# Kernel tuning notes

Measured on AMD Instinct MI355X. Metric: run time of the kernel, lower is better.

Reference implementation:

```python
import jax, jax.numpy as jnp
import numpy as np

B, T, D = 4, 8192, 1024
H = 16
HD = D // H  # 64
TOP_K = 64


def setup_inputs() -> dict:
    key = jax.random.key(0)
    ks = jax.random.split(key, 6)
    x = jax.random.normal(ks[0], (B, T, D), dtype=jnp.float32)
    # torch nn.Linear weights are [out, in]; y = x @ W.T
    Wq = jax.random.normal(ks[1], (D, D), dtype=jnp.float32) * 0.02
    Wk = jax.random.normal(ks[2], (D, D), dtype=jnp.float32) * 0.02
    Wv = jax.random.normal(ks[3], (D, D), dtype=jnp.float32) * 0.02
    Wo = jax.random.normal(ks[4], (D, D), dtype=jnp.float32) * 0.02
    # indexer: nn.Linear(head_dim, 1, bias=False) -> weight [1, HD]; keep as [HD]
    w_score = jax.random.normal(ks[5], (HD,), dtype=jnp.float32) * 0.02
    return {"x": x, "Wq": Wq, "Wk": Wk, "Wv": Wv, "Wo": Wo, "w_score": w_score}


def reference(x, Wq, Wk, Wv, Wo, w_score):
    b, t, d = x.shape
    top_k = min(TOP_K, t)
    # projections: [B,T,D] -> [B,H,T,HD]
    def proj(W):
        return jnp.einsum('btd,ed->bte', x, W).reshape(b, t, H, HD).transpose(0, 2, 1, 3)
    q = proj(Wq)
    k = proj(Wk)
    v = proj(Wv)
    # lightning indexer scores: [B,H,T]
    idx_scores = jnp.einsum('bhtd,d->bht', k, w_score)
    _, top_idx = jax.lax.top_k(idx_scores, top_k)  # [B,H,K]
    idx = top_idx[..., None]  # [B,H,K,1]
    k_sparse = jnp.take_along_axis(k, idx, axis=2)  # [B,H,K,HD]
    v_sparse = jnp.take_along_axis(v, idx, axis=2)
    scale = HD ** -0.5
    scores = jnp.einsum('bhtd,bhkd->bhtk', q, k_sparse) * scale  # [B,H,T,K]
    attn = jax.nn.softmax(scores, axis=-1)
    out = jnp.einsum('bhtk,bhkd->bhtd', attn, v_sparse)  # [B,H,T,HD]
    out = out.transpose(0, 2, 1, 3).reshape(b, t, d)
    return jnp.einsum('btd,ed->bte', out, Wo)
```

## Files before the change

kernel.cpp:

```cpp
#include <hip/hip_runtime.h>
#include <hip/hip_bf16.h>
#include <stdint.h>

#define NB 4
#define NT 8192
#define ND 1024
#define NH 16
#define NHD 64
#define NK 64
#define NM (NB*NT)

typedef __attribute__((ext_vector_type(4))) float f32x4;
typedef __attribute__((ext_vector_type(8))) short s16x8;
typedef const void __attribute__((address_space(1)))* gas1_t;
typedef void __attribute__((address_space(3)))* las3_t;

__device__ __forceinline__ float bf2f(ushort u) {
  union { uint32_t i; float f; } v; v.i = ((uint32_t)u) << 16; return v.f;
}
__device__ __forceinline__ ushort f2bf(float f) {
  union { float f; uint32_t i; } v; v.f = f;
  uint32_t r = v.i + 0x7FFFu + ((v.i >> 16) & 1u);
  return (ushort)(r >> 16);
}
__device__ __forceinline__ uint32_t f2ord(uint32_t u) {
  return (u & 0x80000000u) ? ~u : (u | 0x80000000u);
}

__global__ __launch_bounds__(256) void convert_w_kernel(
    const float* __restrict__ Wq, const float* __restrict__ Wk,
    const float* __restrict__ Wv, const float* __restrict__ Wo,
    const float* __restrict__ wscore,
    ushort* __restrict__ wqb, ushort* __restrict__ wkb,
    ushort* __restrict__ wvb, ushort* __restrict__ wob,
    ushort* __restrict__ uhi, ushort* __restrict__ ulo) {
  int i = blockIdx.x * 256 + threadIdx.x;
  wqb[i] = f2bf(Wq[i]); wkb[i] = f2bf(Wk[i]);
  wvb[i] = f2bf(Wv[i]); wob[i] = f2bf(Wo[i]);
  if (blockIdx.x < 64) {
    int e = (blockIdx.x & 3) * 256 + threadIdx.x;
    int h = blockIdx.x >> 2;
    float acc = 0.f;
    #pragma unroll 8
    for (int d = 0; d < NHD; ++d) acc += wscore[d] * Wk[(size_t)(h*NHD + d)*ND + e];
    ushort hv = f2bf(acc);
    uhi[h*ND + e] = hv;
    ulo[h*ND + e] = f2bf(acc - bf2f(hv));
  }
}

__global__ __launch_bounds__(256) void prep_x_kernel(
    const float* __restrict__ x, const ushort* __restrict__ uhi,
    const ushort* __restrict__ ulo, ushort* __restrict__ xb,
    float* __restrict__ scores) {
  __shared__ __align__(16) ushort Ahi[32 * 128];
  __shared__ __align__(16) ushort Alo[32 * 128];
  __shared__ float red[4][2][16][17];
  int t = threadIdx.x, w = t >> 6, l = t & 63;
  int tok0 = blockIdx.x * 32;
  int srow = t >> 3;
  int sg = (t & 7) * 2;
  int rs = l & 15, ks8 = (l >> 4) * 8;
  f32x4 acc[2];
  acc[0] = (f32x4){0.f,0.f,0.f,0.f};
  acc[1] = (f32x4){0.f,0.f,0.f,0.f};
  for (int kc = 0; kc < 8; ++kc) {
    int kb = kc * 128;
    {
      const float* xr = x + (size_t)(tok0 + srow) * ND + kb + sg * 8;
      f32x4 v0 = *(const f32x4*)xr;
      f32x4 v1 = *(const f32x4*)(xr + 4);
      f32x4 v2 = *(const f32x4*)(xr + 8);
      f32x4 v3 = *(const f32x4*)(xr + 12);
      s16x8 hi0, lo0, hi1, lo1;
      #pragma unroll
      for (int j = 0; j < 4; ++j) {
        ushort h;
        h = f2bf(v0[j]); hi0[j]   = (short)h; lo0[j]   = (short)f2bf(v0[j] - bf2f(h));
        h = f2bf(v1[j]); hi0[4+j] = (short)h; lo0[4+j] = (short)f2bf(v1[j] - bf2f(h));
        h = f2bf(v2[j]); hi1[j]   = (short)h; lo1[j]   = (short)f2bf(v2[j] - bf2f(h));
        h = f2bf(v3[j]); hi1[4+j] = (short)h; lo1[4+j] = (short)f2bf(v3[j] - bf2f(h));
      }
      ushort* xo = xb + (size_t)(tok0 + srow) * ND + kb + sg * 8;
      *(s16x8*)xo = hi0;
      *(s16x8*)(xo + 8) = hi1;
      int p0 = (sg ^ (srow & 7)) * 8, p1 = ((sg + 1) ^ (srow & 7)) * 8;
      *(s16x8*)&Ahi[srow*128 + p0] = hi0;
      *(s16x8*)&Ahi[srow*128 + p1] = hi1;
      *(s16x8*)&Alo[srow*128 + p0] = lo0;
      *(s16x8*)&Alo[srow*128 + p1] = lo1;
    }
    __syncthreads();
    {
      s16x8 bh = *(const s16x8*)(uhi + rs * ND + kb + w * 32 + ks8);
      s16x8 bl = *(const s16x8*)(ulo + rs * ND + kb + w * 32 + ks8);
      int gl = w * 4 + (l >> 4);
      #pragma unroll
      for (int mi = 0; mi < 2; ++mi) {
        int row = mi * 16 + rs;
        int gp = (gl ^ (row & 7)) * 8;
        s16x8 ah = *(const s16x8*)&Ahi[row*128 + gp];
        s16x8 al = *(const s16x8*)&Alo[row*128 + gp];
        acc[mi] = __builtin_amdgcn_mfma_f32_16x16x32_bf16(ah, bh, acc[mi], 0, 0, 0);
        acc[mi] = __builtin_amdgcn_mfma_f32_16x16x32_bf16(al, bh, acc[mi], 0, 0, 0);
        acc[mi] = __builtin_amdgcn_mfma_f32_16x16x32_bf16(ah, bl, acc[mi], 0, 0, 0);
      }
    }
    __syncthreads();
  }
  #pragma unroll
  for (int mi = 0; mi < 2; ++mi)
    #pragma unroll
    for (int r = 0; r < 4; ++r)
      red[w][mi][(l >> 4) * 4 + r][l & 15] = acc[mi][r];
  __syncthreads();
  int boff = ((tok0 >> 13) << 4);
  int tt0 = tok0 & (NT - 1);
  #pragma unroll
  for (int it = 0; it < 2; ++it) {
    int tok = t & 31, h = (t >> 5) + it * 8;
    int mi = tok >> 4, row = tok & 15;
    float s = red[0][mi][row][h] + red[1][mi][row][h]
            + red[2][mi][row][h] + red[3][mi][row][h];
    scores[(size_t)(boff + h) * NT + tt0 + tok] = s;
  }
}

__global__ __launch_bounds__(256) void topsel_kv_kernel(
    const float* __restrict__ scores, const ushort* __restrict__ xb,
    const ushort* __restrict__ wkb, const ushort* __restrict__ wvb,
    ushort* __restrict__ ksp, ushort* __restrict__ vtsp) {
  int bh = blockIdx.x, t = threadIdx.x;
  int b = bh >> 4, h = bh & 15;
  __shared__ uint32_t keys[NT];
  __shared__ int hist[4096];
  __shared__ uint32_t ck[512];
  __shared__ int ci[512];
  __shared__ int chunksum[256];
  __shared__ int s_binB, s_c0;
  __shared__ int cnt_hi, cnt_cand;
  __shared__ int kid[64];
  __shared__ __align__(16) ushort Xs[64 * 128];
  __shared__ __align__(16) ushort Ws[2][64 * 128];

  for (int i = t; i < 4096; i += 256) hist[i] = 0;
  if (t == 0) { cnt_hi = 0; cnt_cand = 0; }
  __syncthreads();
  const uint4* sg = (const uint4*)(scores + (size_t)bh * NT);
  for (int i = t; i < NT/4; i += 256) {
    uint4 v = sg[i];
    uint32_t k0 = f2ord(v.x), k1 = f2ord(v.y), k2 = f2ord(v.z), k3 = f2ord(v.w);
    keys[i*4+0] = k0; keys[i*4+1] = k1; keys[i*4+2] = k2; keys[i*4+3] = k3;
    atomicAdd(&hist[k0 >> 20], 1); atomicAdd(&hist[k1 >> 20], 1);
    atomicAdd(&hist[k2 >> 20], 1); atomicAdd(&hist[k3 >> 20], 1);
  }
  __syncthreads();
  {
    int hi = 4095 - t * 16;
    int s = 0;
    #pragma unroll
    for (int j = 0; j < 16; ++j) s += hist[hi - j];
    chunksum[t] = s;
  }
  __syncthreads();
  if (t == 0) {
    int cum = 0, c = 0;
    while (cum + chunksum[c] < NK) { cum += chunksum[c]; ++c; }
    int bin = 4095 - c * 16;
    while (cum + hist[bin] < NK) { cum += hist[bin]; --bin; }
    s_binB = bin; s_c0 = cum;
  }
  __syncthreads();
  int binB = s_binB, c0 = s_c0;
  for (int i = t; i < NT; i += 256) {
    int bb = keys[i] >> 20;
    if (bb > binB) {
      int p = atomicAdd(&cnt_hi, 1);
      kid[p] = i;
    } else if (bb == binB) {
      int p = atomicAdd(&cnt_cand, 1);
      if (p < 512) { ck[p] = keys[i]; ci[p] = i; }
    }
  }
  __syncthreads();
  int nc = cnt_cand; if (nc > 512) nc = 512;
  int need = NK - c0;
  for (int p = t; p < nc; p += 256) {
    uint32_t myk = ck[p]; int myi = ci[p];
    int rank = 0;
    for (int j = 0; j < nc; ++j) {
      uint32_t kj = ck[j];
      rank += (kj > myk || (kj == myk && ci[j] < myi)) ? 1 : 0;
    }
    if (rank < need) kid[c0 + rank] = myi;
  }

  int w = t >> 6, l = t & 63;
  int sel = w >> 1, nb = (w & 1) * 32;
  f32x4 acc[4][2];
  #pragma unroll
  for (int mi = 0; mi < 4; ++mi)
    #pragma unroll
    for (int ni = 0; ni < 2; ++ni) acc[mi][ni] = (f32x4){0.f,0.f,0.f,0.f};
  int srow = t >> 2;
  int gj = (t & 3) * 4;
  for (int kc = 0; kc < ND; kc += 128) {
    __syncthreads();
    const ushort* xr  = xb  + (size_t)(b*NT + kid[srow]) * ND + kc;
    const ushort* wkr = wkb + (size_t)(h*NHD + srow) * ND + kc;
    const ushort* wvr = wvb + (size_t)(h*NHD + srow) * ND + kc;
    #pragma unroll
    for (int j = 0; j < 4; ++j) {
      int p = ((gj + j) ^ (srow & 7)) * 8;
      *(uint4*)&Xs[srow*128 + p]    = *(const uint4*)(xr  + (gj + j) * 8);
      *(uint4*)&Ws[0][srow*128 + p] = *(const uint4*)(wkr + (gj + j) * 8);
      *(uint4*)&Ws[1][srow*128 + p] = *(const uint4*)(wvr + (gj + j) * 8);
    }
    __syncthreads();
    #pragma unroll
    for (int ks = 0; ks < 4; ++ks) {
      s16x8 bfr[2], afr[4];
      #pragma unroll
      for (int ni = 0; ni < 2; ++ni) {
        int row = nb + ni*16 + (l & 15);
        bfr[ni] = *(const s16x8*)&Ws[sel][row*128 + ((ks*4 + (l >> 4)) ^ (row & 7))*8];
      }
      #pragma unroll
      for (int mi = 0; mi < 4; ++mi) {
        int row = mi*16 + (l & 15);
        afr[mi] = *(const s16x8*)&Xs[row*128 + ((ks*4 + (l >> 4)) ^ (row & 7))*8];
      }
      #pragma unroll
      for (int mi = 0; mi < 4; ++mi)
        #pragma unroll
        for (int ni = 0; ni < 2; ++ni)
          acc[mi][ni] = __builtin_amdgcn_mfma_f32_16x16x32_bf16(
              afr[mi], bfr[ni], acc[mi][ni], 0, 0, 0);
    }
  }
  #pragma unroll
  for (int mi = 0; mi < 4; ++mi)
    #pragma unroll
    for (int ni = 0; ni < 2; ++ni) {
      int d = nb + ni*16 + (l & 15);
      int key0 = mi*16 + (l >> 4)*4;
      if (sel == 0) {
        #pragma unroll
        for (int r = 0; r < 4; ++r)
          ksp[((size_t)bh*NK + key0 + r)*NHD + d] = f2bf(acc[mi][ni][r]);
      } else {
        ushort4 o;
        o.x = f2bf(acc[mi][ni][0]); o.y = f2bf(acc[mi][ni][1]);
        o.z = f2bf(acc[mi][ni][2]); o.w = f2bf(acc[mi][ni][3]);
        *(ushort4*)&vtsp[((size_t)bh*NHD + d)*NK + key0] = o;
      }
    }
}

template<int STORE_BF16>
__global__ __launch_bounds__(512, 2) void gemm8_kernel(
    const ushort* __restrict__ A, const ushort* __restrict__ Bw,
    void* __restrict__ Cout) {
  __shared__ __align__(16) char lds[131072];
  const int t = threadIdx.x, wid = t >> 6, l = t & 63;
  const int wr = wid >> 2, wc = wid & 3;
  int bid = blockIdx.x;
  int wg = (bid & 7) * 64 + (bid >> 3);
  int tm = wg >> 2, tn = wg & 3;
  const int K = 1024, N = 1024;
  const ushort* Ab = A + (size_t)tm * 256 * K;
  const ushort* Bb = Bw + (size_t)tn * 256 * K;
  const int skh  = ((l & 3) * 8) ^ (((l >> 5) & 1) << 4);
  const int srow = l >> 2;
  const int lane_off = (l & 15) * 64 + ((((l >> 4) * 8) ^ (((l >> 3) & 1) << 4)) * 2);
  f32x4 acc[8][4];
  #pragma unroll
  for (int i = 0; i < 8; ++i)
    #pragma unroll
    for (int j = 0; j < 4; ++j) acc[i][j] = (f32x4){0.f, 0.f, 0.f, 0.f};
  s16x8 afr[4][2], bfr[2][2];

#define STG(gbase, matoff, half, ktile, buf) do { \
    const ushort* _s = (gbase) + (size_t)((half)*128 + wid*16 + srow) * K + (ktile)*64 + skh; \
    int _d = (buf)*65536 + (matoff) + ((half)*128 + wid*16)*64; \
    __builtin_amdgcn_global_load_lds((gas1_t)_s, (las3_t)(lds + _d), 16, 0, 0); \
    __builtin_amdgcn_global_load_lds((gas1_t)(_s + 32), (las3_t)(lds + _d + 16384), 16, 0, 0); \
  } while (0)

#define RD_A(mh, kh, buf) do { \
    _Pragma("unroll") \
    for (int mi = 0; mi < 4; ++mi) \
      afr[mi][kh] = *(const s16x8*)(lds + (buf)*65536 + (kh)*16384 + \
                      ((((mh)*2 + wr)*64 + mi*16))*64 + lane_off); \
  } while (0)

#define RD_B(nh, kh, buf) do { \
    _Pragma("unroll") \
    for (int ni = 0; ni < 2; ++ni) \
      bfr[ni][kh] = *(const s16x8*)(lds + (buf)*65536 + 32768 + (kh)*16384 + \
                      (((nh)*128 + wc*32 + ni*16))*64 + lane_off); \
  } while (0)

#define MMAQH(mh, nh, kh) do { \
    __builtin_amdgcn_s_setprio(1); \
    _Pragma("unroll") \
    for (int mi = 0; mi < 4; ++mi) \
      _Pragma("unroll") \
      for (int ni = 0; ni < 2; ++ni) \
        acc[(mh)*4+mi][(nh)*2+ni] = __builtin_amdgcn_mfma_f32_16x16x32_bf16( \
            afr[mi][kh], bfr[ni][kh], acc[(mh)*4+mi][(nh)*2+ni], 0, 0, 0); \
    __builtin_amdgcn_s_setprio(0); \
  } while (0)

#define LG0() do { asm volatile("s_waitcnt lgkmcnt(0)" ::: "memory"); \
                   __builtin_amdgcn_sched_barrier(0); } while (0)
#define ENDPH() do { __builtin_amdgcn_sched_barrier(0); \
                     __builtin_amdgcn_s_barrier(); } while (0)

#define TILE(kt, bc, bn) do { \
  LG0(); MMAQH(0,0,0); RD_A(0,1,bc); RD_B(0,1,bc); ENDPH(); \
  LG0(); MMAQH(0,0,1); RD_B(1,0,bc); \
  if ((kt)+1 < 16) STG(Bb,32768,0,(kt)+1,bn); ENDPH(); \
  LG0(); MMAQH(0,1,0); RD_B(1,1,bc); ENDPH(); \
  LG0(); MMAQH(0,1,1); RD_A(1,0,bc); \
  if ((kt)+2 < 16) STG(Ab,0,0,(kt)+2,bc); ENDPH(); \
  LG0(); MMAQH(1,1,0); RD_A(1,1,bc); ENDPH(); \
  LG0(); MMAQH(1,1,1); RD_B(0,0,bc); \
  if ((kt)+2 < 16) STG(Bb,32768,1,(kt)+2,bc); ENDPH(); \
  LG0(); MMAQH(1,0,0); RD_B(0,1,bc); ENDPH(); \
  LG0(); MMAQH(1,0,1); \
  if ((kt) < 14)       { asm volatile("s_waitcnt vmcnt(4)" ::: "memory"); } \
  else if ((kt) == 14) { asm volatile("s_waitcnt vmcnt(0)" ::: "memory"); } \
  __builtin_amdgcn_sched_barrier(0); \
  __builtin_amdgcn_s_barrier(); \
  if ((kt)+1 < 16) { RD_A(0,0,bn); RD_B(0,0,bn); } \
  if ((kt)+2 < 16) STG(Ab,0,1,(kt)+2,bc); \
} while (0)

  STG(Ab,0,0,0,0); STG(Bb,32768,0,0,0); STG(Ab,0,1,0,0); STG(Bb,32768,1,0,0);
  STG(Ab,0,0,1,1); STG(Bb,32768,1,1,1); STG(Ab,0,1,1,1);
  asm volatile("s_waitcnt vmcnt(6)" ::: "memory");
  __builtin_amdgcn_s_barrier();
  RD_A(0,0,0); RD_B(0,0,0);

  for (int k2 = 0; k2 < 8; ++k2) {
    TILE(2*k2,     0, 1);
    TILE(2*k2 + 1, 1, 0);
  }
#undef TILE
#undef STG
#undef RD_A
#undef RD_B
#undef MMAQH
#undef LG0
#undef ENDPH

  #pragma unroll
  for (int mi8 = 0; mi8 < 8; ++mi8) {
    int grow = tm*256 + (((mi8 >> 2)*2 + wr)*64) + (mi8 & 3)*16 + (l >> 4)*4;
    #pragma unroll
    for (int ni4 = 0; ni4 < 4; ++ni4) {
      int gcol = tn*256 + (ni4 >> 1)*128 + wc*32 + (ni4 & 1)*16 + (l & 15);
      #pragma unroll
      for (int r = 0; r < 4; ++r) {
        size_t off = (size_t)(grow + r) * N + gcol;
        if (STORE_BF16) ((ushort*)Cout)[off] = f2bf(acc[mi8][ni4][r]);
        else            ((float*)Cout)[off]  = acc[mi8][ni4][r];
      }
    }
  }
}

__global__ __launch_bounds__(256, 2) void attn_kernel(
    const ushort* __restrict__ qg, const ushort* __restrict__ ksp,
    const ushort* __restrict__ vtsp, ushort* __restrict__ aout) {
  int bh = blockIdx.y;
  int b = bh >> 4, h = bh & 15;
  int t = threadIdx.x, w = t >> 6, l = t & 63;
  __shared__ __align__(16) ushort Pl[4][1024];
  const ushort* kb = ksp + (size_t)bh * NK * NHD;
  const ushort* vb = vtsp + (size_t)bh * NHD * NK;
  s16x8 kf[2][4], vf[2][4];
  #pragma unroll
  for (int ks = 0; ks < 2; ++ks)
    #pragma unroll
    for (int ni = 0; ni < 4; ++ni) {
      kf[ks][ni] = *(const s16x8*)&kb[(size_t)(ni*16 + (l & 15))*NHD + ks*32 + (l >> 4)*8];
      vf[ks][ni] = *(const s16x8*)&vb[(size_t)(ni*16 + (l & 15))*NK + ks*32 + (l >> 4)*8];
    }
  int rowbase = blockIdx.x * 256 + w * 64;
  #pragma unroll 1
  for (int mi = 0; mi < 4; ++mi) {
    int r0 = rowbase + mi * 16;
    s16x8 af[2];
    #pragma unroll
    for (int ks = 0; ks < 2; ++ks)
      af[ks] = *(const s16x8*)&qg[(size_t)(b*NT + r0 + (l & 15))*ND + h*NHD + ks*32 + (l >> 4)*8];
    f32x4 sc[4];
    #pragma unroll
    for (int ni = 0; ni < 4; ++ni) {
      f32x4 z; z[0]=0.f; z[1]=0.f; z[2]=0.f; z[3]=0.f;
      z = __builtin_amdgcn_mfma_f32_16x16x32_bf16(af[0], kf[0][ni], z, 0, 0, 0);
      sc[ni] = __builtin_amdgcn_mfma_f32_16x16x32_bf16(af[1], kf[1][ni], z, 0, 0, 0);
    }
    #pragma unroll
    for (int r = 0; r < 4; ++r) {
      float v0 = sc[0][r]*0.125f, v1 = sc[1][r]*0.125f;
      float v2 = sc[2][r]*0.125f, v3 = sc[3][r]*0.125f;
      float m = fmaxf(fmaxf(v0, v1), fmaxf(v2, v3));
      #pragma unroll
      for (int mm = 8; mm >= 1; mm >>= 1) m = fmaxf(m, __shfl_xor(m, mm, 64));
      float e0 = __expf(v0 - m), e1 = __expf(v1 - m);
      float e2 = __expf(v2 - m), e3 = __expf(v3 - m);
      float s = e0 + e1 + e2 + e3;
      #pragma unroll
      for (int mm = 8; mm >= 1; mm >>= 1) s += __shfl_xor(s, mm, 64);
      float inv = 1.f / s;
      int prow = (l >> 4)*4 + r;
      int lo = l & 7, hb = (l >> 3) & 1, sw = prow & 7;
      Pl[w][prow*64 + ((0 + hb) ^ sw)*8 + lo] = f2bf(e0 * inv);
      Pl[w][prow*64 + ((2 + hb) ^ sw)*8 + lo] = f2bf(e1 * inv);
      Pl[w][prow*64 + ((4 + hb) ^ sw)*8 + lo] = f2bf(e2 * inv);
      Pl[w][prow*64 + ((6 + hb) ^ sw)*8 + lo] = f2bf(e3 * inv);
    }
    s16x8 pf[2];
    #pragma unroll
    for (int ks = 0; ks < 2; ++ks)
      pf[ks] = *(const s16x8*)&Pl[w][(l & 15)*64 + ((ks*4 + (l >> 4)) ^ (l & 7))*8];
    f32x4 oc[4];
    #pragma unroll
    for (int ni = 0; ni < 4; ++ni) {
      f32x4 z; z[0]=0.f; z[1]=0.f; z[2]=0.f; z[3]=0.f;
      z = __builtin_amdgcn_mfma_f32_16x16x32_bf16(pf[0], vf[0][ni], z, 0, 0, 0);
      oc[ni] = __builtin_amdgcn_mfma_f32_16x16x32_bf16(pf[1], vf[1][ni], z, 0, 0, 0);
    }
    #pragma unroll
    for (int ni = 0; ni < 4; ++ni)
      #pragma unroll
      for (int r = 0; r < 4; ++r) {
        int row = r0 + (l >> 4)*4 + r;
        aout[(size_t)(b*NT + row)*ND + h*NHD + ni*16 + (l & 15)] = f2bf(oc[ni][r]);
      }
  }
}

extern "C" void kernel_launch(void* const* d_in, const int* in_sizes, int n_in,
                              void* d_out, int out_size, void* d_ws, size_t ws_size,
                              hipStream_t stream) {
  (void)in_sizes; (void)n_in; (void)out_size; (void)ws_size;
  const float* x  = (const float*)d_in[0];
  const float* Wq = (const float*)d_in[1];
  const float* Wk = (const float*)d_in[2];
  const float* Wv = (const float*)d_in[3];
  const float* Wo = (const float*)d_in[4];
  const float* wscore = (const float*)d_in[5];

  char* base = (char*)d_ws;
  ushort* xb     = (ushort*)(base + 0);
  ushort* qb     = (ushort*)(base + 67108864);
  float*  scores = (float*) (base + 134217728);
  ushort* uhi    = (ushort*)(base + 136314880);
  ushort* ulo    = (ushort*)(base + 136347648);
  ushort* wqb    = (ushort*)(base + 136380416);
  ushort* wkb    = (ushort*)(base + 138477568);
  ushort* wvb    = (ushort*)(base + 140574720);
  ushort* wob    = (ushort*)(base + 142671872);
  ushort* ksp    = (ushort*)(base + 144785408);
  ushort* vtsp   = (ushort*)(base + 145309696);
  ushort* aout   = xb;

  convert_w_kernel<<<dim3(4096), dim3(256), 0, stream>>>(
      Wq, Wk, Wv, Wo, wscore, wqb, wkb, wvb, wob, uhi, ulo);
  prep_x_kernel<<<dim3(1024), dim3(256), 0, stream>>>(x, uhi, ulo, xb, scores);
  topsel_kv_kernel<<<dim3(64), dim3(256), 0, stream>>>(scores, xb, wkb, wvb, ksp, vtsp);
  gemm8_kernel<1><<<dim3(512), dim3(512), 0, stream>>>(xb, wqb, (void*)qb);
  attn_kernel<<<dim3(32, 64), dim3(256), 0, stream>>>(qb, ksp, vtsp, aout);
  gemm8_kernel<0><<<dim3(512), dim3(512), 0, stream>>>(aout, wob, d_out);
}
```

Baseline: 263.2 us.

## Store Q and attention output in head-major layout between GEMMs and attention

The Q projection GEMM now writes its output in a [B,H,T,HD] head-major layout, and the attention kernel reads Q and writes its output contiguously per head. The output GEMM reads its A operand from that head-major layout. The aim is to replace strided 16-byte accesses across 2 KB rows in the attention kernel with contiguous per-head streams. In exchange, the GEMM epilogue and A-tile staging use more complex addressing, and the GEMM's global stores become scattered across head planes.

```diff
diff --git a/kernel.cpp b/kernel.cpp
--- a/kernel.cpp
+++ b/kernel.cpp
@@ -9,6 +9,7 @@
 #define NHD 64
 #define NK 64
 #define NM (NB*NT)
+#define HMSZ ((size_t)NT * NHD)
 
 typedef __attribute__((ext_vector_type(4))) float f32x4;
 typedef __attribute__((ext_vector_type(8))) short s16x8;
@@ -257,7 +258,7 @@
     }
 }
 
-template<int STORE_BF16>
+template<int STORE_BF16, int A_HM, int C_HM>
 __global__ __launch_bounds__(512, 2) void gemm8_kernel(
     const ushort* __restrict__ A, const ushort* __restrict__ Bw,
     void* __restrict__ Cout) {
@@ -268,7 +269,7 @@
   int wg = (bid & 7) * 64 + (bid >> 3);
   int tm = wg >> 2, tn = wg & 3;
   const int K = 1024, N = 1024;
-  const ushort* Ab = A + (size_t)tm * 256 * K;
+  const ushort* Ab = A + (A_HM ? 0 : (size_t)tm * 256 * K);
   const ushort* Bb = Bw + (size_t)tn * 256 * K;
   const int skh  = ((l & 3) * 8) ^ (((l >> 5) & 1) << 4);
   const int srow = l >> 2;
@@ -280,9 +281,22 @@
     for (int j = 0; j < 4; ++j) acc[i][j] = (f32x4){0.f, 0.f, 0.f, 0.f};
   s16x8 afr[4][2], bfr[2][2];
 
-#define STG(gbase, matoff, half, ktile, buf) do { \
-    const ushort* _s = (gbase) + (size_t)((half)*128 + wid*16 + srow) * K + (ktile)*64 + skh; \
-    int _d = (buf)*65536 + (matoff) + ((half)*128 + wid*16)*64; \
+#define STGA(half, ktile, buf) do { \
+    const ushort* _s; \
+    if (A_HM) { \
+      int _r = tm*256 + (half)*128 + wid*16 + srow; \
+      _s = Ab + ((size_t)((_r >> 13)*16 + (ktile)))*HMSZ + (size_t)(_r & (NT-1))*64 + skh; \
+    } else { \
+      _s = Ab + (size_t)((half)*128 + wid*16 + srow) * K + (ktile)*64 + skh; \
+    } \
+    int _d = (buf)*65536 + ((half)*128 + wid*16)*64; \
+    __builtin_amdgcn_global_load_lds((gas1_t)_s, (las3_t)(lds + _d), 16, 0, 0); \
+    __builtin_amdgcn_global_load_lds((gas1_t)(_s + 32), (las3_t)(lds + _d + 16384), 16, 0, 0); \
+  } while (0)
+
+#define STGB(half, ktile, buf) do { \
+    const ushort* _s = Bb + (size_t)((half)*128 + wid*16 + srow) * K + (ktile)*64 + skh; \
+    int _d = (buf)*65536 + 32768 + ((half)*128 + wid*16)*64; \
     __builtin_amdgcn_global_load_lds((gas1_t)_s, (las3_t)(lds + _d), 16, 0, 0); \
     __builtin_amdgcn_global_load_lds((gas1_t)(_s + 32), (las3_t)(lds + _d + 16384), 16, 0, 0); \
   } while (0)
@@ -320,13 +334,13 @@
 #define TILE(kt, bc, bn) do { \
   LG0(); MMAQH(0,0,0); RD_A(0,1,bc); RD_B(0,1,bc); ENDPH(); \
   LG0(); MMAQH(0,0,1); RD_B(1,0,bc); \
-  if ((kt)+1 < 16) STG(Bb,32768,0,(kt)+1,bn); ENDPH(); \
+  if ((kt)+1 < 16) STGB(0,(kt)+1,bn); ENDPH(); \
   LG0(); MMAQH(0,1,0); RD_B(1,1,bc); ENDPH(); \
   LG0(); MMAQH(0,1,1); RD_A(1,0,bc); \
-  if ((kt)+2 < 16) STG(Ab,0,0,(kt)+2,bc); ENDPH(); \
+  if ((kt)+2 < 16) STGA(0,(kt)+2,bc); ENDPH(); \
   LG0(); MMAQH(1,1,0); RD_A(1,1,bc); ENDPH(); \
   LG0(); MMAQH(1,1,1); RD_B(0,0,bc); \
-  if ((kt)+2 < 16) STG(Bb,32768,1,(kt)+2,bc); ENDPH(); \
+  if ((kt)+2 < 16) STGB(1,(kt)+2,bc); ENDPH(); \
   LG0(); MMAQH(1,0,0); RD_B(0,1,bc); ENDPH(); \
   LG0(); MMAQH(1,0,1); \
   if ((kt) < 14)       { asm volatile("s_waitcnt vmcnt(4)" ::: "memory"); } \
@@ -334,11 +348,11 @@
   __builtin_amdgcn_sched_barrier(0); \
   __builtin_amdgcn_s_barrier(); \
   if ((kt)+1 < 16) { RD_A(0,0,bn); RD_B(0,0,bn); } \
-  if ((kt)+2 < 16) STG(Ab,0,1,(kt)+2,bc); \
+  if ((kt)+2 < 16) STGA(1,(kt)+2,bc); \
 } while (0)
 
-  STG(Ab,0,0,0,0); STG(Bb,32768,0,0,0); STG(Ab,0,1,0,0); STG(Bb,32768,1,0,0);
-  STG(Ab,0,0,1,1); STG(Bb,32768,1,1,1); STG(Ab,0,1,1,1);
+  STGA(0,0,0); STGB(0,0,0); STGA(1,0,0); STGB(1,0,0);
+  STGA(0,1,1); STGB(1,1,1); STGA(1,1,1);
   asm volatile("s_waitcnt vmcnt(6)" ::: "memory");
   __builtin_amdgcn_s_barrier();
   RD_A(0,0,0); RD_B(0,0,0);
@@ -348,7 +362,8 @@
     TILE(2*k2 + 1, 1, 0);
   }
 #undef TILE
-#undef STG
+#undef STGA
+#undef STGB
 #undef RD_A
 #undef RD_B
 #undef MMAQH
@@ -363,7 +378,11 @@
       int gcol = tn*256 + (ni4 >> 1)*128 + wc*32 + (ni4 & 1)*16 + (l & 15);
       #pragma unroll
       for (int r = 0; r < 4; ++r) {
-        size_t off = (size_t)(grow + r) * N + gcol;
+        int rr = grow + r;
+        size_t off;
+        if (C_HM) off = ((size_t)((rr >> 13)*16 + (gcol >> 6)))*HMSZ
+                      + (size_t)(rr & (NT-1))*64 + (gcol & 63);
+        else      off = (size_t)rr * N + gcol;
         if (STORE_BF16) ((ushort*)Cout)[off] = f2bf(acc[mi8][ni4][r]);
         else            ((float*)Cout)[off]  = acc[mi8][ni4][r];
       }
@@ -372,14 +391,15 @@
 }
 
 __global__ __launch_bounds__(256, 2) void attn_kernel(
-    const ushort* __restrict__ qg, const ushort* __restrict__ ksp,
-    const ushort* __restrict__ vtsp, ushort* __restrict__ aout) {
+    const ushort* __restrict__ qhm, const ushort* __restrict__ ksp,
+    const ushort* __restrict__ vtsp, ushort* __restrict__ ahm) {
   int bh = blockIdx.y;
-  int b = bh >> 4, h = bh & 15;
   int t = threadIdx.x, w = t >> 6, l = t & 63;
   __shared__ __align__(16) ushort Pl[4][1024];
   const ushort* kb = ksp + (size_t)bh * NK * NHD;
   const ushort* vb = vtsp + (size_t)bh * NHD * NK;
+  const ushort* qp = qhm + (size_t)bh * HMSZ;
+  ushort* ap = ahm + (size_t)bh * HMSZ;
   s16x8 kf[2][4], vf[2][4];
   #pragma unroll
   for (int ks = 0; ks < 2; ++ks)
@@ -395,7 +415,7 @@
     s16x8 af[2];
     #pragma unroll
     for (int ks = 0; ks < 2; ++ks)
-      af[ks] = *(const s16x8*)&qg[(size_t)(b*NT + r0 + (l & 15))*ND + h*NHD + ks*32 + (l >> 4)*8];
+      af[ks] = *(const s16x8*)&qp[(size_t)(r0 + (l & 15))*NHD + ks*32 + (l >> 4)*8];
     f32x4 sc[4];
     #pragma unroll
     for (int ni = 0; ni < 4; ++ni) {
@@ -439,7 +459,7 @@
       #pragma unroll
       for (int r = 0; r < 4; ++r) {
         int row = r0 + (l >> 4)*4 + r;
-        aout[(size_t)(b*NT + row)*ND + h*NHD + ni*16 + (l & 15)] = f2bf(oc[ni][r]);
+        ap[(size_t)row*NHD + ni*16 + (l & 15)] = f2bf(oc[ni][r]);
       }
   }
 }
@@ -473,7 +493,7 @@
       Wq, Wk, Wv, Wo, wscore, wqb, wkb, wvb, wob, uhi, ulo);
   prep_x_kernel<<<dim3(1024), dim3(256), 0, stream>>>(x, uhi, ulo, xb, scores);
   topsel_kv_kernel<<<dim3(64), dim3(256), 0, stream>>>(scores, xb, wkb, wvb, ksp, vtsp);
-  gemm8_kernel<1><<<dim3(512), dim3(512), 0, stream>>>(xb, wqb, (void*)qb);
+  gemm8_kernel<1, 0, 1><<<dim3(512), dim3(512), 0, stream>>>(xb, wqb, (void*)qb);
   attn_kernel<<<dim3(32, 64), dim3(256), 0, stream>>>(qb, ksp, vtsp, aout);
-  gemm8_kernel<0><<<dim3(512), dim3(512), 0, stream>>>(aout, wob, d_out);
-}
+  gemm8_kernel<0, 1, 0><<<dim3(512), dim3(512), 0, stream>>>(aout, wob, d_out);
+}
```

Measured after the change: 264.4 us. Within noise of the previous version (+0.4%).

## Fuse sparse attention into the Q-projection GEMM epilogue

Applied to the files above, without the earlier changes.

The Q projection GEMM no longer writes Q to global memory. Each block stages its 256x256 Q tile (four heads) in LDS and runs the top-k sparse attention for those heads right away, writing only the attention output. This removes the Q write and read round trip (64 MB bf16) and one kernel launch. The cost is a longer epilogue in a kernel limited to 2 blocks per CU, plus extra LDS traffic and barriers.

```diff
diff --git a/kernel.cpp b/kernel.cpp
--- a/kernel.cpp
+++ b/kernel.cpp
@@ -257,10 +257,11 @@
     }
 }
 
-template<int STORE_BF16>
+template<int FUSE_ATTN>
 __global__ __launch_bounds__(512, 2) void gemm8_kernel(
     const ushort* __restrict__ A, const ushort* __restrict__ Bw,
-    void* __restrict__ Cout) {
+    void* __restrict__ Cout,
+    const ushort* __restrict__ ksp, const ushort* __restrict__ vtsp) {
   __shared__ __align__(16) char lds[131072];
   const int t = threadIdx.x, wid = t >> 6, l = t & 63;
   const int wr = wid >> 2, wc = wid & 3;
@@ -355,92 +356,113 @@
 #undef LG0
 #undef ENDPH
 
-  #pragma unroll
-  for (int mi8 = 0; mi8 < 8; ++mi8) {
-    int grow = tm*256 + (((mi8 >> 2)*2 + wr)*64) + (mi8 & 3)*16 + (l >> 4)*4;
-    #pragma unroll
-    for (int ni4 = 0; ni4 < 4; ++ni4) {
-      int gcol = tn*256 + (ni4 >> 1)*128 + wc*32 + (ni4 & 1)*16 + (l & 15);
-      #pragma unroll
-      for (int r = 0; r < 4; ++r) {
-        size_t off = (size_t)(grow + r) * N + gcol;
-        if (STORE_BF16) ((ushort*)Cout)[off] = f2bf(acc[mi8][ni4][r]);
-        else            ((float*)Cout)[off]  = acc[mi8][ni4][r];
-      }
-    }
-  }
-}
-
-__global__ __launch_bounds__(256, 2) void attn_kernel(
-    const ushort* __restrict__ qg, const ushort* __restrict__ ksp,
-    const ushort* __restrict__ vtsp, ushort* __restrict__ aout) {
-  int bh = blockIdx.y;
-  int b = bh >> 4, h = bh & 15;
-  int t = threadIdx.x, w = t >> 6, l = t & 63;
-  __shared__ __align__(16) ushort Pl[4][1024];
-  const ushort* kb = ksp + (size_t)bh * NK * NHD;
-  const ushort* vb = vtsp + (size_t)bh * NHD * NK;
-  s16x8 kf[2][4], vf[2][4];
-  #pragma unroll
-  for (int ks = 0; ks < 2; ++ks)
-    #pragma unroll
-    for (int ni = 0; ni < 4; ++ni) {
-      kf[ks][ni] = *(const s16x8*)&kb[(size_t)(ni*16 + (l & 15))*NHD + ks*32 + (l >> 4)*8];
-      vf[ks][ni] = *(const s16x8*)&vb[(size_t)(ni*16 + (l & 15))*NK + ks*32 + (l >> 4)*8];
-    }
-  int rowbase = blockIdx.x * 256 + w * 64;
-  #pragma unroll 1
-  for (int mi = 0; mi < 4; ++mi) {
-    int r0 = rowbase + mi * 16;
-    s16x8 af[2];
-    #pragma unroll
-    for (int ks = 0; ks < 2; ++ks)
-      af[ks] = *(const s16x8*)&qg[(size_t)(b*NT + r0 + (l & 15))*ND + h*NHD + ks*32 + (l >> 4)*8];
-    f32x4 sc[4];
-    #pragma unroll
-    for (int ni = 0; ni < 4; ++ni) {
-      f32x4 z; z[0]=0.f; z[1]=0.f; z[2]=0.f; z[3]=0.f;
-      z = __builtin_amdgcn_mfma_f32_16x16x32_bf16(af[0], kf[0][ni], z, 0, 0, 0);
-      sc[ni] = __builtin_amdgcn_mfma_f32_16x16x32_bf16(af[1], kf[1][ni], z, 0, 0, 0);
-    }
-    #pragma unroll
-    for (int r = 0; r < 4; ++r) {
-      float v0 = sc[0][r]*0.125f, v1 = sc[1][r]*0.125f;
-      float v2 = sc[2][r]*0.125f, v3 = sc[3][r]*0.125f;
-      float m = fmaxf(fmaxf(v0, v1), fmaxf(v2, v3));
-      #pragma unroll
-      for (int mm = 8; mm >= 1; mm >>= 1) m = fmaxf(m, __shfl_xor(m, mm, 64));
-      float e0 = __expf(v0 - m), e1 = __expf(v1 - m);
-      float e2 = __expf(v2 - m), e3 = __expf(v3 - m);
-      float s = e0 + e1 + e2 + e3;
-      #pragma unroll
-      for (int mm = 8; mm >= 1; mm >>= 1) s += __shfl_xor(s, mm, 64);
-      float inv = 1.f / s;
-      int prow = (l >> 4)*4 + r;
-      int lo = l & 7, hb = (l >> 3) & 1, sw = prow & 7;
-      Pl[w][prow*64 + ((0 + hb) ^ sw)*8 + lo] = f2bf(e0 * inv);
-      Pl[w][prow*64 + ((2 + hb) ^ sw)*8 + lo] = f2bf(e1 * inv);
-      Pl[w][prow*64 + ((4 + hb) ^ sw)*8 + lo] = f2bf(e2 * inv);
-      Pl[w][prow*64 + ((6 + hb) ^ sw)*8 + lo] = f2bf(e3 * inv);
-    }
-    s16x8 pf[2];
-    #pragma unroll
-    for (int ks = 0; ks < 2; ++ks)
-      pf[ks] = *(const s16x8*)&Pl[w][(l & 15)*64 + ((ks*4 + (l >> 4)) ^ (l & 7))*8];
-    f32x4 oc[4];
-    #pragma unroll
-    for (int ni = 0; ni < 4; ++ni) {
-      f32x4 z; z[0]=0.f; z[1]=0.f; z[2]=0.f; z[3]=0.f;
-      z = __builtin_amdgcn_mfma_f32_16x16x32_bf16(pf[0], vf[0][ni], z, 0, 0, 0);
-      oc[ni] = __builtin_amdgcn_mfma_f32_16x16x32_bf16(pf[1], vf[1][ni], z, 0, 0, 0);
-    }
-    #pragma unroll
-    for (int ni = 0; ni < 4; ++ni)
-      #pragma unroll
-      for (int r = 0; r < 4; ++r) {
-        int row = r0 + (l >> 4)*4 + r;
-        aout[(size_t)(b*NT + row)*ND + h*NHD + ni*16 + (l & 15)] = f2bf(oc[ni][r]);
-      }
+  if (!FUSE_ATTN) {
+    #pragma unroll
+    for (int mi8 = 0; mi8 < 8; ++mi8) {
+      int grow = tm*256 + (((mi8 >> 2)*2 + wr)*64) + (mi8 & 3)*16 + (l >> 4)*4;
+      #pragma unroll
+      for (int ni4 = 0; ni4 < 4; ++ni4) {
+        int gcol = tn*256 + (ni4 >> 1)*128 + wc*32 + (ni4 & 1)*16 + (l & 15);
+        #pragma unroll
+        for (int r = 0; r < 4; ++r) {
+          size_t off = (size_t)(grow + r) * N + gcol;
+          ((float*)Cout)[off] = acc[mi8][ni4][r];
+        }
+      }
+    }
+  } else {
+    ushort* Qs = (ushort*)lds;
+    ushort* Pl = (ushort*)(lds + 65536);
+    ushort* ap = (ushort*)Cout;
+    const int hl = wid >> 2, tq = wid & 3;
+    #pragma unroll 1
+    for (int hg = 0; hg < 2; ++hg) {
+      #pragma unroll
+      for (int mi8 = 0; mi8 < 8; ++mi8) {
+        int lrow0 = ((mi8 >> 2)*2 + wr)*64 + (mi8 & 3)*16 + (l >> 4)*4;
+        #pragma unroll
+        for (int nj = 0; nj < 2; ++nj) {
+          int ccol = wc*32 + nj*16 + (l & 15);
+          int colg = ccol >> 3;
+          #pragma unroll
+          for (int r = 0; r < 4; ++r) {
+            int lrow = lrow0 + r;
+            Qs[lrow*128 + ((colg ^ (lrow & 7))*8) + (ccol & 7)] =
+                f2bf(acc[mi8][hg*2 + nj][r]);
+          }
+        }
+      }
+      __syncthreads();
+      int h = tn*4 + hg*2 + hl;
+      int bh2 = ((tm*256) >> 13) * 16 + h;
+      const ushort* kb = ksp + (size_t)bh2 * NK * NHD;
+      const ushort* vb = vtsp + (size_t)bh2 * NHD * NK;
+      s16x8 kf[2][4], vf[2][4];
+      #pragma unroll
+      for (int ks = 0; ks < 2; ++ks)
+        #pragma unroll
+        for (int ni = 0; ni < 4; ++ni) {
+          kf[ks][ni] = *(const s16x8*)&kb[(size_t)(ni*16 + (l & 15))*NHD + ks*32 + (l >> 4)*8];
+          vf[ks][ni] = *(const s16x8*)&vb[(size_t)(ni*16 + (l & 15))*NK + ks*32 + (l >> 4)*8];
+        }
+      #pragma unroll 1
+      for (int mi = 0; mi < 4; ++mi) {
+        int lr0 = tq*64 + mi*16;
+        s16x8 af[2];
+        #pragma unroll
+        for (int ks = 0; ks < 2; ++ks) {
+          int lrow = lr0 + (l & 15);
+          int colg = hl*8 + ks*4 + (l >> 4);
+          af[ks] = *(const s16x8*)&Qs[lrow*128 + ((colg ^ (lrow & 7))*8)];
+        }
+        f32x4 sc[4];
+        #pragma unroll
+        for (int ni = 0; ni < 4; ++ni) {
+          f32x4 z; z[0]=0.f; z[1]=0.f; z[2]=0.f; z[3]=0.f;
+          z = __builtin_amdgcn_mfma_f32_16x16x32_bf16(af[0], kf[0][ni], z, 0, 0, 0);
+          sc[ni] = __builtin_amdgcn_mfma_f32_16x16x32_bf16(af[1], kf[1][ni], z, 0, 0, 0);
+        }
+        #pragma unroll
+        for (int r = 0; r < 4; ++r) {
+          float v0 = sc[0][r]*0.125f, v1 = sc[1][r]*0.125f;
+          float v2 = sc[2][r]*0.125f, v3 = sc[3][r]*0.125f;
+          float m = fmaxf(fmaxf(v0, v1), fmaxf(v2, v3));
+          #pragma unroll
+          for (int mm = 8; mm >= 1; mm >>= 1) m = fmaxf(m, __shfl_xor(m, mm, 64));
+          float e0 = __expf(v0 - m), e1 = __expf(v1 - m);
+          float e2 = __expf(v2 - m), e3 = __expf(v3 - m);
+          float s = e0 + e1 + e2 + e3;
+          #pragma unroll
+          for (int mm = 8; mm >= 1; mm >>= 1) s += __shfl_xor(s, mm, 64);
+          float inv = 1.f / s;
+          int prow = (l >> 4)*4 + r;
+          int lo = l & 7, hb = (l >> 3) & 1, sw = prow & 7;
+          Pl[wid*1024 + prow*64 + ((0 + hb) ^ sw)*8 + lo] = f2bf(e0 * inv);
+          Pl[wid*1024 + prow*64 + ((2 + hb) ^ sw)*8 + lo] = f2bf(e1 * inv);
+          Pl[wid*1024 + prow*64 + ((4 + hb) ^ sw)*8 + lo] = f2bf(e2 * inv);
+          Pl[wid*1024 + prow*64 + ((6 + hb) ^ sw)*8 + lo] = f2bf(e3 * inv);
+        }
+        s16x8 pf[2];
+        #pragma unroll
+        for (int ks = 0; ks < 2; ++ks)
+          pf[ks] = *(const s16x8*)&Pl[wid*1024 + (l & 15)*64 + ((ks*4 + (l >> 4)) ^ (l & 7))*8];
+        f32x4 oc[4];
+        #pragma unroll
+        for (int ni = 0; ni < 4; ++ni) {
+          f32x4 z; z[0]=0.f; z[1]=0.f; z[2]=0.f; z[3]=0.f;
+          z = __builtin_amdgcn_mfma_f32_16x16x32_bf16(pf[0], vf[0][ni], z, 0, 0, 0);
+          oc[ni] = __builtin_amdgcn_mfma_f32_16x16x32_bf16(pf[1], vf[1][ni], z, 0, 0, 0);
+        }
+        #pragma unroll
+        for (int ni = 0; ni < 4; ++ni)
+          #pragma unroll
+          for (int r = 0; r < 4; ++r) {
+            int grow = tm*256 + lr0 + (l >> 4)*4 + r;
+            ap[(size_t)grow*ND + h*NHD + ni*16 + (l & 15)] = f2bf(oc[ni][r]);
+          }
+      }
+      __syncthreads();
+    }
   }
 }
 
@@ -457,7 +479,7 @@
 
   char* base = (char*)d_ws;
   ushort* xb     = (ushort*)(base + 0);
-  ushort* qb     = (ushort*)(base + 67108864);
+  ushort* aout   = (ushort*)(base + 67108864);
   float*  scores = (float*) (base + 134217728);
   ushort* uhi    = (ushort*)(base + 136314880);
   ushort* ulo    = (ushort*)(base + 136347648);
@@ -467,13 +489,11 @@
   ushort* wob    = (ushort*)(base + 142671872);
   ushort* ksp    = (ushort*)(base + 144785408);
   ushort* vtsp   = (ushort*)(base + 145309696);
-  ushort* aout   = xb;
 
   convert_w_kernel<<<dim3(4096), dim3(256), 0, stream>>>(
       Wq, Wk, Wv, Wo, wscore, wqb, wkb, wvb, wob, uhi, ulo);
   prep_x_kernel<<<dim3(1024), dim3(256), 0, stream>>>(x, uhi, ulo, xb, scores);
   topsel_kv_kernel<<<dim3(64), dim3(256), 0, stream>>>(scores, xb, wkb, wvb, ksp, vtsp);
-  gemm8_kernel<1><<<dim3(512), dim3(512), 0, stream>>>(xb, wqb, (void*)qb);
-  attn_kernel<<<dim3(32, 64), dim3(256), 0, stream>>>(qb, ksp, vtsp, aout);
-  gemm8_kernel<0><<<dim3(512), dim3(512), 0, stream>>>(aout, wob, d_out);
-}
+  gemm8_kernel<1><<<dim3(512), dim3(512), 0, stream>>>(xb, wqb, (void*)aout, ksp, vtsp);
+  gemm8_kernel<0><<<dim3(512), dim3(512), 0, stream>>>(aout, wob, d_out, nullptr, nullptr);
+}
```

New measurement: 348.7 us. +32.5%, slower.
